# Kernel tuning notes

Hardware: AMD Instinct MI355X
Metric: run time of the kernel (lower is better)

Reference implementation:

```python
import jax, jax.numpy as jnp
import numpy as np

N_HEADS, D_MODEL, D_K, D_V = 16, 1024, 64, 64
B, S = 2, 2048

def setup_inputs() -> dict:
    key = jax.random.key(0)
    k = jax.random.split(key, 7)
    s = 1.0 / np.sqrt(D_MODEL)
    return {
        "input_Q": jax.random.normal(k[0], (B, S, D_MODEL), jnp.float32),
        "input_K": jax.random.normal(k[1], (B, S, D_MODEL), jnp.float32),
        "input_V": jax.random.normal(k[2], (B, S, D_MODEL), jnp.float32),
        "W_Q": jax.random.normal(k[3], (D_MODEL, N_HEADS * D_K), jnp.float32) * s,
        "W_K": jax.random.normal(k[4], (D_MODEL, N_HEADS * D_K), jnp.float32) * s,
        "W_V": jax.random.normal(k[5], (D_MODEL, N_HEADS * D_V), jnp.float32) * s,
        "W_O": jax.random.normal(k[6], (N_HEADS * D_V, D_MODEL), jnp.float32) * s,
    }

def reference(input_Q, input_K, input_V, W_Q, W_K, W_V, W_O):
    b = input_Q.shape[0]
    # project and split heads: [b, h, s, d]
    Q = (input_Q @ W_Q).reshape(b, -1, N_HEADS, D_K).transpose(0, 2, 1, 3)
    K = (input_K @ W_K).reshape(b, -1, N_HEADS, D_K).transpose(0, 2, 1, 3)
    V = (input_V @ W_V).reshape(b, -1, N_HEADS, D_V).transpose(0, 2, 1, 3)
    scores = jnp.einsum("bhqd,bhkd->bhqk", Q, K) / np.sqrt(D_K)
    attn = jax.nn.softmax(scores, axis=-1)
    context = jnp.einsum("bhqk,bhkd->bhqd", attn, V)
    context = context.transpose(0, 2, 1, 3).reshape(b, -1, N_HEADS * D_V)
    out = context @ W_O + input_Q  # residual
    # LayerNorm instantiated fresh in torch forward -> gamma=1, beta=0
    mu = jnp.mean(out, axis=-1, keepdims=True)
    var = jnp.var(out, axis=-1, keepdims=True)
    return (out - mu) / jnp.sqrt(var + 1e-5)
```

## Files before the change

### kernel.cpp

```cpp
#include <hip/hip_runtime.h>
#include <hip/hip_bf16.h>
#include <cstdint>
#include <cstddef>

#define DEVFN __device__ __forceinline__

typedef __attribute__((ext_vector_type(8))) short short8;
typedef __attribute__((ext_vector_type(4))) float f32x4;
typedef __attribute__((ext_vector_type(16))) float f32x16;
typedef __attribute__((ext_vector_type(4))) unsigned short us4;
typedef __attribute__((ext_vector_type(2))) unsigned int u32x2;

static constexpr int S_LEN = 2048;
static constexpr int DM    = 1024;
static constexpr int H     = 16;
static constexpr int DK    = 64;
static constexpr int BATCH = 2;
static constexpr int MROWS = BATCH * S_LEN;

DEVFN unsigned short f2bf(float f) {
  union { float f; unsigned int u; } x; x.f = f;
  unsigned int r = x.u + 0x7fffu + ((x.u >> 16) & 1u);
  return (unsigned short)(r >> 16);
}

DEVFN float fast_exp2(float x) { return __builtin_amdgcn_exp2f(x); }

DEVFN f32x4 mfma16(short8 a, short8 b, f32x4 c) {
  return __builtin_amdgcn_mfma_f32_16x16x32_bf16(a, b, c, 0, 0, 0);
}

DEVFN f32x16 mfma32(short8 a, short8 b, f32x16 c) {
  return __builtin_amdgcn_mfma_f32_32x32x16_bf16(a, b, c, 0, 0, 0);
}

DEVFN unsigned int cvtpk(float lo, float hi) {
  unsigned int r;
  asm("v_cvt_pk_bf16_f32 %0, %1, %2" : "=v"(r) : "v"(lo), "v"(hi));
  return r;
}

DEVFN void plswap(unsigned int &a, unsigned int &b) {
  u32x2 r = __builtin_amdgcn_permlane32_swap(a, b, false, false);
  a = r[0]; b = r[1];
}

DEVFN void gload_lds16(const void* g, void* l) {
  __builtin_amdgcn_global_load_lds(
      (const __attribute__((address_space(1))) void*)g,
      (__attribute__((address_space(3))) void*)l, 16, 0, 0);
}

__global__ __launch_bounds__(256) void wt_transpose(
    const float* __restrict__ Wq, const float* __restrict__ Wk,
    const float* __restrict__ Wv, const float* __restrict__ Wo,
    unsigned short* __restrict__ Tq, unsigned short* __restrict__ Tk,
    unsigned short* __restrict__ Tv, unsigned short* __restrict__ To)
{
  const float* W = blockIdx.z == 0 ? Wq : blockIdx.z == 1 ? Wk : blockIdx.z == 2 ? Wv : Wo;
  unsigned short* T = blockIdx.z == 0 ? Tq : blockIdx.z == 1 ? Tk : blockIdx.z == 2 ? Tv : To;
  __shared__ float tile[32][33];
  int n0 = blockIdx.x * 32, k0 = blockIdx.y * 32;
  int tx = threadIdx.x & 31, ty = threadIdx.x >> 5;
#pragma unroll
  for (int i = 0; i < 4; ++i)
    tile[ty + 8 * i][tx] = W[(size_t)(k0 + ty + 8 * i) * DM + n0 + tx];
  __syncthreads();
#pragma unroll
  for (int i = 0; i < 4; ++i) {
    int n = ty + 8 * i;
    T[(size_t)(n0 + n) * DM + k0 + tx] = f2bf(tile[tx][n]);
  }
}

__global__ __launch_bounds__(256) void xcvt3(
    const float* __restrict__ X0, const float* __restrict__ X1,
    const float* __restrict__ X2, unsigned short* __restrict__ Y)
{
  const float* X = blockIdx.y == 0 ? X0 : blockIdx.y == 1 ? X1 : X2;
  unsigned short* Yz = Y + (size_t)blockIdx.y * MROWS * DM;
  const size_t i = ((size_t)blockIdx.x * 256 + threadIdx.x) * 8;
  float4 v0 = *(const float4*)(X + i);
  float4 v1 = *(const float4*)(X + i + 4);
  union { us4 u[2]; short8 s; } r;
  r.u[0].x = f2bf(v0.x); r.u[0].y = f2bf(v0.y); r.u[0].z = f2bf(v0.z); r.u[0].w = f2bf(v0.w);
  r.u[1].x = f2bf(v1.x); r.u[1].y = f2bf(v1.y); r.u[1].z = f2bf(v1.z); r.u[1].w = f2bf(v1.w);
  *(short8*)(Yz + i) = r.s;
}

__global__ __launch_bounds__(256, 3) void gemm_qkv(
    const unsigned short* __restrict__ Xb,
    const unsigned short* __restrict__ Tq, const unsigned short* __restrict__ Tk,
    const unsigned short* __restrict__ Tv,
    unsigned short* __restrict__ Qb, unsigned short* __restrict__ Kb,
    unsigned short* __restrict__ Vt)
{
  __shared__ __align__(16) unsigned short As[2][128 * 32];
  __shared__ __align__(16) unsigned short Bs[2][128 * 32];

  const int z = blockIdx.z;
  const unsigned short* A = Xb + (size_t)z * MROWS * DM;
  const unsigned short* T = z == 0 ? Tq : z == 1 ? Tk : Tv;

  const int tid = threadIdx.x;
  const int lane = tid & 63, w = tid >> 6;
  const int wm = w >> 1, wn = w & 1;
  const int lr = lane & 15, lg = lane >> 4;
  const int m0 = blockIdx.x * 128, n0 = blockIdx.y * 128;

  const int srw = lane >> 2, sch = lane & 3;

  auto stage = [&](int buf, int k0) {
#pragma unroll
    for (int i = 0; i < 2; ++i) {
      const int rr = (w * 2 + i) * 16 + srw;
      const int sc = (sch ^ ((rr >> 1) & 3)) * 8;
      gload_lds16(A + (size_t)(m0 + rr) * DM + k0 + sc, &As[buf][(w * 2 + i) * 512]);
      gload_lds16(T + (size_t)(n0 + rr) * DM + k0 + sc, &Bs[buf][(w * 2 + i) * 512]);
    }
  };

  f32x4 acc[4][4];
#pragma unroll
  for (int m = 0; m < 4; ++m)
#pragma unroll
    for (int n = 0; n < 4; ++n) acc[m][n] = (f32x4){0.f, 0.f, 0.f, 0.f};

  stage(0, 0);

  int buf = 0;
  for (int kt = 0; kt < DM / 32; ++kt) {
    if (kt + 1 < DM / 32) {
      stage(buf ^ 1, (kt + 1) * 32);
      asm volatile("s_waitcnt vmcnt(4)");
    } else {
      asm volatile("s_waitcnt vmcnt(0)");
    }
    __builtin_amdgcn_s_barrier();

    short8 af[4], bfr[4];
#pragma unroll
    for (int m = 0; m < 4; ++m) {
      const int row = wm * 64 + m * 16 + lr;
      const int ch = lg ^ ((row >> 1) & 3);
      af[m] = *(const short8*)&As[buf][row * 32 + ch * 8];
    }
#pragma unroll
    for (int n = 0; n < 4; ++n) {
      const int row = wn * 64 + n * 16 + lr;
      const int ch = lg ^ ((row >> 1) & 3);
      bfr[n] = *(const short8*)&Bs[buf][row * 32 + ch * 8];
    }
#pragma unroll
    for (int m = 0; m < 4; ++m)
#pragma unroll
      for (int n = 0; n < 4; ++n) acc[m][n] = mfma16(af[m], bfr[n], acc[m][n]);

    __builtin_amdgcn_s_barrier();
    buf ^= 1;
  }

  if (z < 2) {
    const float scale = (z == 0) ? 0.125f * 1.44269504088896f : 1.0f;
    unsigned short* out = z == 0 ? Qb : Kb;
#pragma unroll
    for (int m = 0; m < 4; ++m)
#pragma unroll
      for (int n = 0; n < 4; ++n) {
        int col = n0 + wn * 64 + n * 16 + lr;
        int h = col >> 6, d = col & 63;
#pragma unroll
        for (int r = 0; r < 4; ++r) {
          int row = m0 + wm * 64 + m * 16 + lg * 4 + r;
          int b = row >> 11, s = row & (S_LEN - 1);
          out[((size_t)(b * H + h) * S_LEN + s) * DK + d] = f2bf(acc[m][n][r] * scale);
        }
      }
  } else {
#pragma unroll
    for (int m = 0; m < 4; ++m)
#pragma unroll
      for (int n = 0; n < 4; ++n) {
        int col = n0 + wn * 64 + n * 16 + lr;
        int h = col >> 6, d = col & 63;
        int row = m0 + wm * 64 + m * 16 + lg * 4;
        int b = row >> 11, s = row & (S_LEN - 1);
        us4 u;
#pragma unroll
        for (int r = 0; r < 4; ++r) u[r] = f2bf(acc[m][n][r]);
        *(us4*)(Vt + ((size_t)(b * H + h) * DK + d) * S_LEN + s) = u;
      }
  }
}

__global__ __launch_bounds__(512, 4) void attn(
    const unsigned short* __restrict__ Qg, const unsigned short* __restrict__ Kg,
    const unsigned short* __restrict__ Vg, unsigned short* __restrict__ ctx)
{
  constexpr int KBLK = 64;
  __shared__ __align__(16) unsigned char smem[65536];

  const int tid = threadIdx.x, lane = tid & 63, w = tid >> 6;
  const int wg = w >> 2, w4 = w & 3;
  const int l31 = lane & 31, hi = lane >> 5;

  const int orig = blockIdx.x;
  const int id = (orig & 7) * 64 + (orig >> 3);
  const int bh = id >> 4, qb = id & 15;
  const int b = bh >> 4, h = bh & 15;
  const int q = qb * 128 + w4 * 32 + l31;
  const int t0 = wg * 16;

  const unsigned short* Qbh = Qg + (size_t)bh * S_LEN * DK;
  const unsigned short* Kbh = Kg + (size_t)bh * S_LEN * DK;
  const unsigned short* Vbh = Vg + (size_t)bh * DK * S_LEN;

  const int srow = lane >> 3;
  const int sslot = ((lane & 7) ^ srow) * 8;

  auto Kbuf = [&](int buf) { return (unsigned short*)(smem + (size_t)(wg * 2 + buf) * 16384); };
  auto Vbuf = [&](int buf) { return (unsigned short*)(smem + (size_t)(wg * 2 + buf) * 16384 + 8192); };

  auto stage = [&](int buf, int t) {
    const int kbase = t * KBLK;
    unsigned short* kb = Kbuf(buf);
    unsigned short* vb = Vbuf(buf);
#pragma unroll
    for (int c = 0; c < 2; ++c) {
      const int rbase = w4 * 8 + c * 32;
      gload_lds16(Kbh + (size_t)(kbase + rbase + srow) * DK + sslot, kb + rbase * DK);
      gload_lds16(Vbh + (size_t)(rbase + srow) * S_LEN + kbase + sslot, vb + rbase * DK);
    }
  };

  short8 qf[4];
#pragma unroll
  for (int kk = 0; kk < 4; ++kk)
    qf[kk] = *(const short8*)(Qbh + (size_t)q * DK + kk * 16 + hi * 8);

  f32x16 o0, o1;
#pragma unroll
  for (int i = 0; i < 16; ++i) { o0[i] = 0.f; o1[i] = 0.f; }
  float lrun = 0.f;

  const int swz = (l31 & 7) << 4;

  auto tile = [&](int buf) {
    const char* Kb = (const char*)Kbuf(buf);
    const char* Vb = (const char*)Vbuf(buf);

    f32x16 s0, s1;
#pragma unroll
    for (int i = 0; i < 16; ++i) { s0[i] = 0.f; s1[i] = 0.f; }
    __builtin_amdgcn_s_setprio(1);
#pragma unroll
    for (int kk = 0; kk < 4; ++kk) {
      const int cb = (kk * 32 + hi * 16) ^ swz;
      short8 ka0 = *(const short8*)(Kb + l31 * 128 + cb);
      short8 ka1 = *(const short8*)(Kb + (32 + l31) * 128 + cb);
      s0 = mfma32(ka0, qf[kk], s0);
      s1 = mfma32(ka1, qf[kk], s1);
    }
    __builtin_amdgcn_s_setprio(0);

#pragma unroll
    for (int i = 0; i < 16; ++i) {
      s0[i] = fast_exp2(s0[i]);
      s1[i] = fast_exp2(s1[i]);
    }

    float d0[16];
#pragma unroll
    for (int i = 0; i < 16; ++i) d0[i] = s0[i] + s1[i];
#pragma unroll
    for (int st = 8; st >= 1; st >>= 1)
#pragma unroll
      for (int i = 0; i < st; ++i) d0[i] = d0[i] + d0[i + st];
    lrun += d0[0] + __shfl_xor(d0[0], 32, 64);

    short8 pf[4];
#pragma unroll
    for (int sl = 0; sl < 4; ++sl) {
      const f32x16& sv = (sl & 2) ? s1 : s0;
      const int base = (sl & 1) * 8;
      unsigned int w0 = cvtpk(sv[base + 0], sv[base + 1]);
      unsigned int w1 = cvtpk(sv[base + 2], sv[base + 3]);
      unsigned int w2 = cvtpk(sv[base + 4], sv[base + 5]);
      unsigned int w3 = cvtpk(sv[base + 6], sv[base + 7]);
      plswap(w0, w2);
      plswap(w1, w3);
      union { unsigned int u[4]; short8 v; } pu;
      pu.u[0] = w0; pu.u[1] = w1; pu.u[2] = w2; pu.u[3] = w3;
      pf[sl] = pu.v;
    }

    __builtin_amdgcn_s_setprio(1);
#pragma unroll
    for (int sl = 0; sl < 4; ++sl) {
      const int cb = (sl * 32 + hi * 16) ^ swz;
      short8 va0 = *(const short8*)(Vb + l31 * 128 + cb);
      short8 va1 = *(const short8*)(Vb + (32 + l31) * 128 + cb);
      o0 = mfma32(va0, pf[sl], o0);
      o1 = mfma32(va1, pf[sl], o1);
    }
    __builtin_amdgcn_s_setprio(0);
  };

  stage(0, t0);

  int buf = 0;
  for (int tt = 0; tt < 16; ++tt) {
    if (tt + 1 < 16) {
      stage(buf ^ 1, t0 + tt + 1);
      asm volatile("s_waitcnt vmcnt(4)");
    } else {
      asm volatile("s_waitcnt vmcnt(0)");
    }
    __builtin_amdgcn_s_barrier();
    tile(buf);
    __builtin_amdgcn_s_barrier();
    buf ^= 1;
  }

  __syncthreads();
  float* cmb = (float*)smem;
  if (wg == 1) {
    float* dst = cmb + ((size_t)(w4 * 64 + lane)) * 33;
#pragma unroll
    for (int i = 0; i < 16; ++i) { dst[i] = o0[i]; dst[16 + i] = o1[i]; }
    dst[32] = lrun;
  }
  __syncthreads();
  if (wg == 0) {
    const float* src = cmb + ((size_t)(w4 * 64 + lane)) * 33;
#pragma unroll
    for (int i = 0; i < 16; ++i) { o0[i] += src[i]; o1[i] += src[16 + i]; }
    lrun += src[32];

    const float rinv = 1.0f / lrun;
    unsigned short* crow = ctx + ((size_t)(b * S_LEN + q)) * DM + h * DK;
#pragma unroll
    for (int n = 0; n < 2; ++n) {
#pragma unroll
      for (int r = 0; r < 16; r += 2) {
        const float v0 = (n ? o1[r] : o0[r]) * rinv;
        const float v1 = (n ? o1[r + 1] : o0[r + 1]) * rinv;
        const int d = (r & 3) + 8 * (r >> 2) + 4 * hi + 32 * n;
        *(unsigned int*)(crow + d) = cvtpk(v0, v1);
      }
    }
  }
}

__global__ __launch_bounds__(256, 3) void gemm_out(
    const unsigned short* __restrict__ C, const unsigned short* __restrict__ To,
    const float* __restrict__ resid, float* __restrict__ y)
{
  __shared__ __align__(16) unsigned short As[2][128 * 32];
  __shared__ __align__(16) unsigned short Bs[2][64 * 32];

  const int tid = threadIdx.x;
  const int lane = tid & 63, w = tid >> 6;
  const int wm = w >> 1, wn = w & 1;
  const int lr = lane & 15, lg = lane >> 4;
  const int m0 = blockIdx.x * 128, n0 = blockIdx.y * 64;

  const int brr = lane >> 2, bsc = lane & 3;

  auto stage = [&](int buf, int k0) {
#pragma unroll
    for (int i = 0; i < 2; ++i) {
      const int rr = (w * 2 + i) * 16 + brr;
      const int sc = (bsc ^ ((rr >> 1) & 3)) * 8;
      gload_lds16(C + (size_t)(m0 + rr) * DM + k0 + sc, &As[buf][(w * 2 + i) * 512]);
    }
    const int rr = w * 16 + brr;
    const int sc = (bsc ^ ((rr >> 1) & 3)) * 8;
    gload_lds16(To + (size_t)(n0 + rr) * DM + k0 + sc, &Bs[buf][w * 512]);
  };

  f32x4 acc[4][2];
#pragma unroll
  for (int m = 0; m < 4; ++m)
#pragma unroll
    for (int n = 0; n < 2; ++n) acc[m][n] = (f32x4){0.f, 0.f, 0.f, 0.f};

  stage(0, 0);

  int buf = 0;
  for (int kt = 0; kt < DM / 32; ++kt) {
    if (kt + 1 < DM / 32) {
      stage(buf ^ 1, (kt + 1) * 32);
      asm volatile("s_waitcnt vmcnt(3)");
    } else {
      asm volatile("s_waitcnt vmcnt(0)");
    }
    __builtin_amdgcn_s_barrier();

    short8 af[4], bfr[2];
#pragma unroll
    for (int m = 0; m < 4; ++m) {
      const int row = wm * 64 + m * 16 + lr;
      const int ch = lg ^ ((row >> 1) & 3);
      af[m] = *(const short8*)&As[buf][row * 32 + ch * 8];
    }
#pragma unroll
    for (int n = 0; n < 2; ++n) {
      const int row = wn * 32 + n * 16 + lr;
      const int ch = lg ^ ((row >> 1) & 3);
      bfr[n] = *(const short8*)&Bs[buf][row * 32 + ch * 8];
    }
#pragma unroll
    for (int m = 0; m < 4; ++m)
#pragma unroll
      for (int n = 0; n < 2; ++n) acc[m][n] = mfma16(af[m], bfr[n], acc[m][n]);

    __builtin_amdgcn_s_barrier();
    buf ^= 1;
  }

#pragma unroll
  for (int m = 0; m < 4; ++m)
#pragma unroll
    for (int n = 0; n < 2; ++n) {
      int col = n0 + wn * 32 + n * 16 + lr;
#pragma unroll
      for (int r = 0; r < 4; ++r) {
        int row = m0 + wm * 64 + m * 16 + lg * 4 + r;
        size_t idx = (size_t)row * DM + col;
        y[idx] = acc[m][n][r] + resid[idx];
      }
    }
}

__global__ __launch_bounds__(256) void lnorm(const float* __restrict__ y, float* __restrict__ out)
{
  const int row = blockIdx.x;
  const int tid = threadIdx.x;
  const float4 v = ((const float4*)(y + (size_t)row * DM))[tid];
  float s = v.x + v.y + v.z + v.w;
  float sq = v.x * v.x + v.y * v.y + v.z * v.z + v.w * v.w;
  s += __shfl_xor(s, 1, 64);  sq += __shfl_xor(sq, 1, 64);
  s += __shfl_xor(s, 2, 64);  sq += __shfl_xor(sq, 2, 64);
  s += __shfl_xor(s, 4, 64);  sq += __shfl_xor(sq, 4, 64);
  s += __shfl_xor(s, 8, 64);  sq += __shfl_xor(sq, 8, 64);
  s += __shfl_xor(s, 16, 64); sq += __shfl_xor(sq, 16, 64);
  s += __shfl_xor(s, 32, 64); sq += __shfl_xor(sq, 32, 64);
  __shared__ float ps[4], pq[4];
  int w = tid >> 6, lane = tid & 63;
  if (lane == 0) { ps[w] = s; pq[w] = sq; }
  __syncthreads();
  s = ps[0] + ps[1] + ps[2] + ps[3];
  sq = pq[0] + pq[1] + pq[2] + pq[3];
  float mean = s * (1.0f / DM);
  float var = sq * (1.0f / DM) - mean * mean;
  float rstd = rsqrtf(var + 1e-5f);
  float4 ov;
  ov.x = (v.x - mean) * rstd;
  ov.y = (v.y - mean) * rstd;
  ov.z = (v.z - mean) * rstd;
  ov.w = (v.w - mean) * rstd;
  ((float4*)(out + (size_t)row * DM))[tid] = ov;
}

extern "C" void kernel_launch(void* const* d_in, const int* in_sizes, int n_in,
                              void* d_out, int out_size, void* d_ws, size_t ws_size,
                              hipStream_t stream) {
  const float* Xq = (const float*)d_in[0];
  const float* Xk = (const float*)d_in[1];
  const float* Xv = (const float*)d_in[2];
  const float* Wq = (const float*)d_in[3];
  const float* Wk = (const float*)d_in[4];
  const float* Wv = (const float*)d_in[5];
  const float* Wo = (const float*)d_in[6];
  float* out = (float*)d_out;
  char* ws = (char*)d_ws;

  const size_t WT_BYTES  = (size_t)DM * DM * 2;
  const size_t XB_BYTES  = (size_t)3 * MROWS * DM * 2;
  const size_t QKV_BYTES = (size_t)BATCH * H * S_LEN * DK * 2;

  size_t off = 0;
  auto take = [&](size_t bytes) { size_t o = off; off += (bytes + 255) & ~(size_t)255; return o; };
  unsigned short* Tq  = (unsigned short*)(ws + take(WT_BYTES));
  unsigned short* Tk  = (unsigned short*)(ws + take(WT_BYTES));
  unsigned short* Tv  = (unsigned short*)(ws + take(WT_BYTES));
  unsigned short* To  = (unsigned short*)(ws + take(WT_BYTES));
  size_t xb_off = take(XB_BYTES);
  unsigned short* Xb  = (unsigned short*)(ws + xb_off);
  unsigned short* Qb  = (unsigned short*)(ws + take(QKV_BYTES));
  unsigned short* Kb  = (unsigned short*)(ws + take(QKV_BYTES));
  unsigned short* Vt  = (unsigned short*)(ws + take(QKV_BYTES));
  unsigned short* Ctx = Xb;
  float* y = (float*)(ws + xb_off + (size_t)MROWS * DM * 2);

  if (ws_size < off) return;

  wt_transpose<<<dim3(32, 32, 4), 256, 0, stream>>>(Wq, Wk, Wv, Wo, Tq, Tk, Tv, To);
  xcvt3<<<dim3(2048, 3), 256, 0, stream>>>(Xq, Xk, Xv, Xb);
  gemm_qkv<<<dim3(32, 8, 3), 256, 0, stream>>>(Xb, Tq, Tk, Tv, Qb, Kb, Vt);
  attn<<<dim3(512), 512, 0, stream>>>(Qb, Kb, Vt, Ctx);
  gemm_out<<<dim3(32, 16), 256, 0, stream>>>(Ctx, To, Xq, y);
  lnorm<<<MROWS, 256, 0, stream>>>(y, out);
}
```

Before: 122.3 us.

## Load V fragments directly from global memory instead of staging through LDS

V tiles are no longer copied into shared memory. Each lane now reads its V operand fragments for the PV MFMAs straight from global memory, which halves the LDS footprint (allowing higher occupancy) and removes the LDS write/read traffic for V. The launch-bounds occupancy hint is dropped and the vmcnt wait is adjusted for the smaller number of async loads. The risk is global-load latency sitting directly in the MFMA dependency chain without double buffering, and less coalesced access to V.

```diff
diff --git a/kernel.cpp b/kernel.cpp
--- a/kernel.cpp
+++ b/kernel.cpp
@@ -193,12 +193,12 @@
   }
 }
 
-__global__ __launch_bounds__(512, 4) void attn(
+__global__ __launch_bounds__(512) void attn(
     const unsigned short* __restrict__ Qg, const unsigned short* __restrict__ Kg,
     const unsigned short* __restrict__ Vg, unsigned short* __restrict__ ctx)
 {
   constexpr int KBLK = 64;
-  __shared__ __align__(16) unsigned char smem[65536];
+  __shared__ __align__(16) unsigned char smem[33792];
 
   const int tid = threadIdx.x, lane = tid & 63, w = tid >> 6;
   const int wg = w >> 2, w4 = w & 3;
@@ -213,23 +213,21 @@
 
   const unsigned short* Qbh = Qg + (size_t)bh * S_LEN * DK;
   const unsigned short* Kbh = Kg + (size_t)bh * S_LEN * DK;
-  const unsigned short* Vbh = Vg + (size_t)bh * DK * S_LEN;
+  const unsigned short* V0g = Vg + (size_t)bh * DK * S_LEN + (size_t)l31 * S_LEN + hi * 8;
+  const unsigned short* V1g = V0g + 32 * S_LEN;
 
   const int srow = lane >> 3;
   const int sslot = ((lane & 7) ^ srow) * 8;
 
-  auto Kbuf = [&](int buf) { return (unsigned short*)(smem + (size_t)(wg * 2 + buf) * 16384); };
-  auto Vbuf = [&](int buf) { return (unsigned short*)(smem + (size_t)(wg * 2 + buf) * 16384 + 8192); };
+  auto Kbuf = [&](int buf) { return (unsigned short*)(smem + (size_t)(wg * 2 + buf) * 8192); };
 
   auto stage = [&](int buf, int t) {
     const int kbase = t * KBLK;
     unsigned short* kb = Kbuf(buf);
-    unsigned short* vb = Vbuf(buf);
 #pragma unroll
     for (int c = 0; c < 2; ++c) {
       const int rbase = w4 * 8 + c * 32;
       gload_lds16(Kbh + (size_t)(kbase + rbase + srow) * DK + sslot, kb + rbase * DK);
-      gload_lds16(Vbh + (size_t)(rbase + srow) * S_LEN + kbase + sslot, vb + rbase * DK);
     }
   };
 
@@ -245,9 +243,8 @@
 
   const int swz = (l31 & 7) << 4;
 
-  auto tile = [&](int buf) {
+  auto tile = [&](int buf, int kbase) {
     const char* Kb = (const char*)Kbuf(buf);
-    const char* Vb = (const char*)Vbuf(buf);
 
     f32x16 s0, s1;
 #pragma unroll
@@ -294,15 +291,24 @@
       pf[sl] = pu.v;
     }
 
+    short8 va00 = *(const short8*)(V0g + kbase + 0 * 16);
+    short8 va10 = *(const short8*)(V1g + kbase + 0 * 16);
+    short8 va01 = *(const short8*)(V0g + kbase + 1 * 16);
+    short8 va11 = *(const short8*)(V1g + kbase + 1 * 16);
+    short8 va02 = *(const short8*)(V0g + kbase + 2 * 16);
+    short8 va12 = *(const short8*)(V1g + kbase + 2 * 16);
+    short8 va03 = *(const short8*)(V0g + kbase + 3 * 16);
+    short8 va13 = *(const short8*)(V1g + kbase + 3 * 16);
+
     __builtin_amdgcn_s_setprio(1);
-#pragma unroll
-    for (int sl = 0; sl < 4; ++sl) {
-      const int cb = (sl * 32 + hi * 16) ^ swz;
-      short8 va0 = *(const short8*)(Vb + l31 * 128 + cb);
-      short8 va1 = *(const short8*)(Vb + (32 + l31) * 128 + cb);
-      o0 = mfma32(va0, pf[sl], o0);
-      o1 = mfma32(va1, pf[sl], o1);
-    }
+    o0 = mfma32(va00, pf[0], o0);
+    o1 = mfma32(va10, pf[0], o1);
+    o0 = mfma32(va01, pf[1], o0);
+    o1 = mfma32(va11, pf[1], o1);
+    o0 = mfma32(va02, pf[2], o0);
+    o1 = mfma32(va12, pf[2], o1);
+    o0 = mfma32(va03, pf[3], o0);
+    o1 = mfma32(va13, pf[3], o1);
     __builtin_amdgcn_s_setprio(0);
   };
 
@@ -312,12 +318,12 @@
   for (int tt = 0; tt < 16; ++tt) {
     if (tt + 1 < 16) {
       stage(buf ^ 1, t0 + tt + 1);
-      asm volatile("s_waitcnt vmcnt(4)");
+      asm volatile("s_waitcnt vmcnt(2)");
     } else {
       asm volatile("s_waitcnt vmcnt(0)");
     }
     __builtin_amdgcn_s_barrier();
-    tile(buf);
+    tile(buf, (t0 + tt) * KBLK);
     __builtin_amdgcn_s_barrier();
     buf ^= 1;
   }
```

Result: slower. 154.8 us (+26.6%).
